# Optimization experiments

Hardware: AMD Instinct MI355X
Metric: run time of the kernel (lower is better)

The kernel has to match this reference:

```python
import jax, jax.numpy as jnp
import numpy as np


def setup_inputs() -> dict:
    key = jax.random.key(0)
    ks = jax.random.split(key, 9)
    b, m, e, d = 4, 4096, 2048, 256
    s = 1.0 / np.sqrt(d)
    return {
        "features": jax.random.normal(ks[0], (b, m, d), jnp.float32),
        "inc_mat": (jax.random.uniform(ks[1], (b, m, e)) < 0.05).astype(jnp.float32),
        "vc_W_att": jax.random.normal(ks[2], (d, d), jnp.float32) * s,
        "vc_W_proj": jax.random.normal(ks[3], (d, d), jnp.float32) * s,
        "vc_alpha": jnp.float32(0.5),
        "ec_W_att": jax.random.normal(ks[4], (d, d), jnp.float32) * s,
        "ec_W_proj": jax.random.normal(ks[5], (d, d), jnp.float32) * s,
        "ec_alpha": jnp.float32(0.5),
        "n_layers": 3,
    }


def _vertex_conv(feat, inc, W_att, W_proj, alpha, prev_edge):
    # feat: [b,m,d], inc: [b,m,e]
    node_scores = jnp.einsum('bmd,kd->bmk', feat, W_att)          # attention Linear (x @ W.T)
    edge_scores = jnp.einsum('bme,bmd->bed', inc, node_scores)    # inc^T @ scores
    attn = jax.nn.softmax(edge_scores, axis=1)                    # softmax over edge dim (dim=1 in torch)
    # einsum('bme,bmd->bmed') then ('bmed,bed->bed') == attn * (inc^T @ feat); no 4D intermediate
    agg = jnp.einsum('bme,bmd->bed', inc, feat)
    ef = jnp.einsum('bed,kd->bek', attn * agg, W_proj)
    if prev_edge is not None:
        ef = alpha * prev_edge + (1.0 - alpha) * ef
    return ef


def _edge_conv(inc, edge_feats, W_proj, alpha, prev_node):
    # note: EdgeConv's attention softmax is computed but unused in the original forward
    weighted = jnp.einsum('bed,bme->bmd', edge_feats, inc)        # scatter edges back to nodes
    nf = jnp.einsum('bmd,kd->bmk', weighted, W_proj)
    if prev_node is not None:
        nf = alpha * prev_node + (1.0 - alpha) * nf
    return nf


def reference(features, inc_mat, vc_W_att, vc_W_proj, vc_alpha, ec_W_att, ec_W_proj, ec_alpha, n_layers):
    edge_feats = _vertex_conv(features, inc_mat, vc_W_att, vc_W_proj, vc_alpha, None)
    node_feats = _edge_conv(inc_mat, edge_feats, ec_W_proj, ec_alpha, features)
    for _ in range(1, int(n_layers)):
        edge_feats = _vertex_conv(features, inc_mat, vc_W_att, vc_W_proj, vc_alpha, edge_feats)
        node_feats = _edge_conv(inc_mat, edge_feats, ec_W_proj, ec_alpha, node_feats)
    return (node_feats, edge_feats, inc_mat)
```

## Files before the change

### kernel.cpp

```cpp
#include <hip/hip_runtime.h>
#include <hip/hip_bf16.h>
#include <math.h>

typedef __attribute__((ext_vector_type(8))) short s8v;
typedef __attribute__((ext_vector_type(4))) float f32x4;

__device__ __forceinline__ ushort f2bf(float x){ __hip_bfloat16 h = __float2bfloat16(x); return *(ushort*)&h; }
__device__ __forceinline__ float  bf2f(ushort u){ return __bfloat162float(*(__hip_bfloat16*)&u); }

__device__ __forceinline__ void gload16(const void* g, void* l) {
  __builtin_amdgcn_global_load_lds(
      (const __attribute__((address_space(1))) void*)g,
      (__attribute__((address_space(3))) void*)l, 16, 0, 0);
}

template<int MAP> __device__ __forceinline__ int kmap(int k){
  if constexpr (MAP==0) return k;
  else if constexpr (MAP==1) return k & 4095;
  else if constexpr (MAP==3) return (((k>>8)&1)<<8) | (k&255);
  else if constexpr (MAP==4) return k & 255;
  else return (((k>>9)&1)<<8) | (k&255);
}

template<int AMAP, int BMAP, int EPI, int FR, int GORD>
__global__ __launch_bounds__(256)
void gemm_kernel(const ushort* __restrict__ A, int lda, long long sA,
                 const ushort* __restrict__ B, int ldb, long long sB,
                 void* __restrict__ Cp, void* __restrict__ Cp2,
                 int ldc, long long sC, int ldc2, long long sC2,
                 long long kpC, int Kloc, int kparts,
                 const float* __restrict__ blend,
                 const float* __restrict__ alpha_p, const int* __restrict__ L_p)
{
  constexpr int BMt = 32*FR;
  __shared__ ushort As[BMt][32];
  __shared__ ushort Bs[BMt][32];

  const int z  = blockIdx.z;
  const int b  = z / kparts;
  const int kp = z - b*kparts;
  const int kbase = kp * Kloc;
  A += (size_t)b * sA;
  B += (size_t)b * sB;
  const int m0 = (GORD ? blockIdx.x : blockIdx.y) * BMt;
  const int n0 = (GORD ? blockIdx.y : blockIdx.x) * BMt;
  const int t = threadIdx.x, lane = t & 63, wid = t >> 6;
  const int wr = (wid>>1)*(16*FR), wc = (wid&1)*(16*FR);
  const int lrow = lane & 15, koff = (lane>>4)<<3;
  const int rsub = lane >> 2;
  const int kc   = (lane & 3) * 8;

  f32x4 acc[FR][FR];
  #pragma unroll
  for (int i=0;i<FR;i++)
    #pragma unroll
    for (int j=0;j<FR;j++) acc[i][j] = (f32x4)(0.f);

  for (int k0 = 0; k0 < Kloc; k0 += 32) {
    #pragma unroll
    for (int c = wid; c < 2*FR; c += 4) {
      const int row = c*16 + rsub;
      gload16(A + (size_t)(m0+row)*lda + kmap<AMAP>(kbase+k0+kc), (char*)&As[0][0] + c*1024);
      gload16(B + (size_t)(n0+row)*ldb + kmap<BMAP>(kbase+k0+kc), (char*)&Bs[0][0] + c*1024);
    }
    __syncthreads();
    s8v af[FR], bfv[FR];
    #pragma unroll
    for (int mi=0; mi<FR; mi++) af[mi]  = *(const s8v*)&As[wr+mi*16+lrow][koff];
    #pragma unroll
    for (int ni=0; ni<FR; ni++) bfv[ni] = *(const s8v*)&Bs[wc+ni*16+lrow][koff];
    #pragma unroll
    for (int mi=0; mi<FR; mi++)
      #pragma unroll
      for (int ni=0; ni<FR; ni++)
        acc[mi][ni] = __builtin_amdgcn_mfma_f32_16x16x32_bf16(af[mi], bfv[ni], acc[mi][ni], 0,0,0);
    __syncthreads();
  }

  float aL = 0.f;
  if constexpr (EPI==2) { aL = powf(*alpha_p, (float)(*L_p)); }
  const int cr = (lane>>4)<<2, cc = lane & 15;
  #pragma unroll
  for (int mi=0; mi<FR; mi++)
    #pragma unroll
    for (int ni=0; ni<FR; ni++) {
      const int row0 = m0 + wr + mi*16 + cr;
      const int col  = n0 + wc + ni*16 + cc;
      if constexpr (EPI==0) {
        float* C = (float*)Cp + kp*kpC + (size_t)b*sC;
        #pragma unroll
        for (int r=0;r<4;r++) C[(size_t)(row0+r)*ldc + col] = acc[mi][ni][r];
      } else if constexpr (EPI==2) {
        float* C = (float*)Cp + (size_t)b*sC;
        const float* bl = blend + (size_t)b*sC;
        #pragma unroll
        for (int r=0;r<4;r++) {
          const size_t idx = (size_t)(row0+r)*ldc + col;
          C[idx] = aL*bl[idx] + (1.f-aL)*acc[mi][ni][r];
        }
      } else if constexpr (EPI==3) {
        float* C = (float*)Cp + (size_t)b*sC;
        ushort* C2 = (ushort*)Cp2 + (size_t)b*sC;
        #pragma unroll
        for (int r=0;r<4;r++) {
          const size_t idx = (size_t)(row0+r)*ldc + col;
          C[idx] = acc[mi][ni][r];
          C2[idx] = f2bf(acc[mi][ni][r]);
        }
      } else if constexpr (EPI==6) {
        float* C = (float*)Cp + (size_t)b*sC;
        #pragma unroll
        for (int r=0;r<4;r++) C[(size_t)(row0+r)*ldc + col] = acc[mi][ni][r];
        float* C2 = (float*)Cp2 + (size_t)b*sC2 + (size_t)col*ldc2 + row0;
        *(f32x4*)C2 = acc[mi][ni];
      } else {
        ushort4 o;
        o.x = f2bf(acc[mi][ni][0]); o.y = f2bf(acc[mi][ni][1]);
        o.z = f2bf(acc[mi][ni][2]); o.w = f2bf(acc[mi][ni][3]);
        *(ushort4*)((ushort*)Cp2 + (size_t)b*sC2 + (size_t)col*ldc2 + row0) = o;
      }
    }
}

__global__ __launch_bounds__(256)
void trans_inc_kernel(const float* __restrict__ src, float* __restrict__ outF32, int writeF32,
                      ushort* __restrict__ incbf, ushort* __restrict__ incT)
{
  __shared__ ushort T[64][65];
  const int b = blockIdx.z, m0 = blockIdx.x*64, e0 = blockIdx.y*64;
  const int t = threadIdx.x, rl = t>>2, cl = (t&3)*16;
  const size_t roff = (size_t)b*4096*2048 + (size_t)(m0+rl)*2048 + e0 + cl;
  const float* s = src + roff;
  ushort tmp[16] __attribute__((aligned(16)));
  float4 vv[4];
  #pragma unroll
  for (int i=0;i<4;i++) {
    vv[i] = ((const float4*)s)[i];
    tmp[4*i+0]=f2bf(vv[i].x); tmp[4*i+1]=f2bf(vv[i].y);
    tmp[4*i+2]=f2bf(vv[i].z); tmp[4*i+3]=f2bf(vv[i].w);
  }
  if (writeF32) {
    float4* o = (float4*)(outF32 + roff);
    #pragma unroll
    for (int i=0;i<4;i++) o[i] = vv[i];
  }
  ushort* d = incbf + roff;
  *(s8v*)d = *(s8v*)&tmp[0]; *(s8v*)(d+8) = *(s8v*)&tmp[8];
  #pragma unroll
  for (int j=0;j<16;j++) T[rl][cl+j] = tmp[j];
  __syncthreads();
  const int er = t>>2, mc = (t&3)*16;
  ushort o[16] __attribute__((aligned(16)));
  #pragma unroll
  for (int j=0;j<16;j++) o[j] = T[mc+j][er];
  ushort* d2 = incT + (size_t)b*2048*4096 + (size_t)(e0+er)*4096 + m0 + mc;
  *(s8v*)d2 = *(s8v*)&o[0]; *(s8v*)(d2+8) = *(s8v*)&o[8];
}

__global__ __launch_bounds__(256)
void trans_feat_kernel(const float* __restrict__ feat, ushort* __restrict__ fT)
{
  __shared__ ushort Th[64][65], Tl[64][65];
  const int b = blockIdx.z, m0 = blockIdx.x*64, d0 = blockIdx.y*64;
  const int t = threadIdx.x, rl = t>>2, cl = (t&3)*16;
  const float* s = feat + (size_t)b*4096*256 + (size_t)(m0+rl)*256 + d0 + cl;
  #pragma unroll
  for (int i=0;i<4;i++) {
    float4 v = ((const float4*)s)[i];
    float a[4] = {v.x,v.y,v.z,v.w};
    #pragma unroll
    for (int j=0;j<4;j++) {
      ushort h = f2bf(a[j]); Th[rl][cl+4*i+j] = h; Tl[rl][cl+4*i+j] = f2bf(a[j] - bf2f(h));
    }
  }
  __syncthreads();
  const int dr = t>>2, mc = (t&3)*16;
  ushort oh[16] __attribute__((aligned(16)));
  ushort ol[16] __attribute__((aligned(16)));
  #pragma unroll
  for (int j=0;j<16;j++) { oh[j] = Th[mc+j][dr]; ol[j] = Tl[mc+j][dr]; }
  ushort* d2 = fT + (size_t)b*256*8192 + (size_t)(d0+dr)*8192 + m0 + mc;
  *(s8v*)d2 = *(s8v*)&oh[0]; *(s8v*)(d2+8) = *(s8v*)&oh[8];
  *(s8v*)(d2+4096) = *(s8v*)&ol[0]; *(s8v*)(d2+4104) = *(s8v*)&ol[8];
}

__global__ __launch_bounds__(256)
void cvt_w_kernel(const float4* __restrict__ W, ushort* __restrict__ Ws)
{
  size_t i  = (size_t)blockIdx.x * 256 + threadIdx.x;
  size_t e0 = i * 4;
  int c = (int)(e0 & 255), r = (int)(e0 >> 8);
  float4 v = W[i];
  float a[4] = {v.x,v.y,v.z,v.w};
  ushort* hi = Ws + (size_t)r*512 + c;
  #pragma unroll
  for (int j=0;j<4;j++) { ushort h = f2bf(a[j]); hi[j] = h; hi[256+j] = f2bf(a[j]-bf2f(h)); }
}

__global__ __launch_bounds__(256)
void aggsum_kernel(const float* __restrict__ parts, long long kpC, int kparts,
                   ushort* __restrict__ AGGcat)
{
  const size_t i4 = (size_t)blockIdx.x*256 + threadIdx.x;
  float4 sv = make_float4(0.f,0.f,0.f,0.f);
  for (int kp=0; kp<kparts; kp++) {
    float4 v = ((const float4*)(parts + (size_t)kp*kpC))[i4];
    sv.x+=v.x; sv.y+=v.y; sv.z+=v.z; sv.w+=v.w;
  }
  const size_t flat = i4*4;
  const size_t row = flat >> 8;
  const int d = (int)(flat & 255);
  float a[4] = {sv.x, sv.y, sv.z, sv.w};
  ushort4 hi, lo;
  { ushort h=f2bf(a[0]); hi.x=h; lo.x=f2bf(a[0]-bf2f(h)); }
  { ushort h=f2bf(a[1]); hi.y=h; lo.y=f2bf(a[1]-bf2f(h)); }
  { ushort h=f2bf(a[2]); hi.z=h; lo.z=f2bf(a[2]-bf2f(h)); }
  { ushort h=f2bf(a[3]); hi.w=h; lo.w=f2bf(a[3]-bf2f(h)); }
  ushort* dst = AGGcat + row*512 + d;
  *(ushort4*)dst = hi; *(ushort4*)(dst+256) = lo;
}

__global__ __launch_bounds__(256)
void stats_kernel(const float* __restrict__ ESt, float2* __restrict__ stats)
{
  const int b = blockIdx.x >> 8, d = blockIdx.x & 255;
  const float* base = ESt + ((size_t)b*256 + d)*2048;
  const int t = threadIdx.x;
  const float4* p = (const float4*)base + t*2;
  float4 x = p[0], y = p[1];
  float v[8] = {x.x,x.y,x.z,x.w,y.x,y.y,y.z,y.w};
  float mx = v[0];
  #pragma unroll
  for (int j=1;j<8;j++) mx = fmaxf(mx, v[j]);
  #pragma unroll
  for (int off=32; off>=1; off>>=1) mx = fmaxf(mx, __shfl_down(mx, off));
  __shared__ float sm[8];
  const int lane = t & 63, w = t >> 6;
  if (lane==0) sm[w] = mx;
  __syncthreads();
  if (t==0) { sm[4] = fmaxf(fmaxf(sm[0],sm[1]),fmaxf(sm[2],sm[3])); }
  __syncthreads();
  mx = sm[4];
  float s = 0.f;
  #pragma unroll
  for (int j=0;j<8;j++) s += __expf(v[j]-mx);
  #pragma unroll
  for (int off=32; off>=1; off>>=1) s += __shfl_down(s, off);
  if (lane==0) sm[w] = s;
  __syncthreads();
  if (t==0) { float ss = sm[0]+sm[1]+sm[2]+sm[3]; stats[blockIdx.x] = make_float2(mx, 1.f/ss); }
}

__global__ __launch_bounds__(256)
void pmul_kernel(const float* __restrict__ ES, const ushort* __restrict__ AGGcat,
                 const float2* __restrict__ stats, ushort* __restrict__ P)
{
  const int b = blockIdx.x >> 6, e0 = (blockIdx.x & 63) * 32;
  const int t = threadIdx.x, tx = t & 63, ty = t >> 6;
  const int d4 = tx*4;
  const float2 st0 = stats[b*256+d4+0], st1 = stats[b*256+d4+1];
  const float2 st2 = stats[b*256+d4+2], st3 = stats[b*256+d4+3];
  for (int e = e0+ty; e < e0+32; e += 4) {
    const size_t ro = (size_t)b*2048 + e;
    float4 es = *(const float4*)(ES + ro*256 + d4);
    ushort4 ah = *(const ushort4*)(AGGcat + ro*512 + d4);
    ushort4 al = *(const ushort4*)(AGGcat + ro*512 + 256 + d4);
    ushort4 o;
    o.x = f2bf(__expf(es.x-st0.x)*st0.y*(bf2f(ah.x)+bf2f(al.x)));
    o.y = f2bf(__expf(es.y-st1.x)*st1.y*(bf2f(ah.y)+bf2f(al.y)));
    o.z = f2bf(__expf(es.z-st2.x)*st2.y*(bf2f(ah.z)+bf2f(al.z)));
    o.w = f2bf(__expf(es.w-st3.x)*st3.y*(bf2f(ah.w)+bf2f(al.w)));
    *(ushort4*)(P + ro*256 + d4) = o;
  }
}

__global__ __launch_bounds__(256)
void inc_copy_kernel(const float4* __restrict__ src, float4* __restrict__ dst, size_t n4)
{
  size_t i = (size_t)blockIdx.x*256 + threadIdx.x;
  const size_t stride = (size_t)gridDim.x*256;
  for (; i < n4; i += stride) dst[i] = src[i];
}

extern "C" void kernel_launch(void* const* d_in, const int* in_sizes, int n_in,
                              void* d_out, int out_size, void* d_ws, size_t ws_size,
                              hipStream_t stream) {
  const float* feat    = (const float*)d_in[0];
  const float* inc     = (const float*)d_in[1];
  const float* vcWatt  = (const float*)d_in[2];
  const float* vcWproj = (const float*)d_in[3];
  const float* ecWproj = (const float*)d_in[6];
  const float* ecAlpha = (const float*)d_in[7];
  const int*   nLayers = (const int*)d_in[8];

  const int Bb=4, Mm=4096, E=2048, D=256;
  const size_t nodeN = (size_t)Bb*Mm*D, edgeN = (size_t)Bb*E*D, incN = (size_t)Bb*Mm*E;

  const int kparts = 8;
  const size_t fTB    = (size_t)Bb*256*8192*2;
  const size_t partsB = (size_t)kparts*Bb*E*D*4;
  const size_t AGGcatB= (size_t)Bb*E*512*2;
  const size_t ESB    = (size_t)Bb*E*D*4;
  const size_t EStB   = ESB;
  const size_t PB     = edgeN*2;
  const size_t ebfB   = edgeN*2;
  const size_t E2TB   = edgeN*2;
  const size_t WsB    = (size_t)3*256*512*2;
  const size_t statB  = (size_t)Bb*256*sizeof(float2);
  const size_t incTB  = incN*2, incbfB = incN*2;
  const size_t needB  = fTB+partsB+AGGcatB+ESB+EStB+PB+ebfB+E2TB+WsB+statB;
  const bool planA = ws_size >= needB + incTB + incbfB;

  char* ws = (char*)d_ws;
  ushort* fT    = (ushort*)ws;  ws += fTB;
  float*  parts = (float*)ws;   ws += partsB;
  ushort* AGGcat= (ushort*)ws;  ws += AGGcatB;
  float*  ES    = (float*)ws;   ws += ESB;
  float*  ESt   = (float*)ws;   ws += EStB;
  ushort* P     = (ushort*)ws;  ws += PB;
  ushort* edgebf= (ushort*)ws;  ws += ebfB;
  ushort* E2T   = (ushort*)ws;  ws += E2TB;
  ushort* Ws0   = (ushort*)ws;
  ushort* Ws1   = Ws0 + 256*512;
  ushort* Ws2   = Ws1 + 256*512;
  ws += WsB;
  float2* stats = (float2*)ws;  ws += statB;

  float* outNode = (float*)d_out;
  float* outEdge = outNode + nodeN;
  float* outInc  = outEdge + edgeN;
  ushort *incT, *incbf;
  if (planA) { incT = (ushort*)ws; incbf = incT + incN; }
  else       { incT = (ushort*)outInc; incbf = incT + incN; }

  const long long kpC = (long long)Bb*E*D;
  dim3 blk(256);

  cvt_w_kernel<<<dim3(64), blk, 0, stream>>>((const float4*)vcWatt,  Ws0);
  cvt_w_kernel<<<dim3(64), blk, 0, stream>>>((const float4*)vcWproj, Ws1);
  cvt_w_kernel<<<dim3(64), blk, 0, stream>>>((const float4*)ecWproj, Ws2);
  trans_feat_kernel<<<dim3(64,4,4), blk, 0, stream>>>(feat, fT);
  trans_inc_kernel<<<dim3(64,32,4), blk, 0, stream>>>(inc, outInc, planA ? 1 : 0, incbf, incT);

  gemm_kernel<1,0,0,4,0><<<dim3(2,16,4*kparts), blk, 0, stream>>>(
      incT, 4096, (long long)E*4096, fT, 8192, (long long)256*8192,
      parts, nullptr, D, (long long)E*D, 0, 0, kpC, 8192/kparts, kparts,
      nullptr, nullptr, nullptr);

  aggsum_kernel<<<dim3(2048), blk, 0, stream>>>(parts, kpC, kparts, AGGcat);

  gemm_kernel<5,3,6,2,0><<<dim3(4,32,4), blk, 0, stream>>>(
      AGGcat, 512, (long long)E*512, Ws0, 512, 0,
      ES, ESt, D, (long long)E*D, E, (long long)D*E, 0, 1024, 1,
      nullptr, nullptr, nullptr);

  stats_kernel<<<dim3(Bb*256), blk, 0, stream>>>(ESt, stats);
  pmul_kernel<<<dim3(Bb*64), blk, 0, stream>>>(ES, AGGcat, stats, P);

  gemm_kernel<4,3,3,2,0><<<dim3(4,32,4), blk, 0, stream>>>(
      P, 256, (long long)E*D, Ws1, 512, 0,
      outEdge, edgebf, D, (long long)E*D, 0, 0, 0, 512, 1,
      nullptr, nullptr, nullptr);

  gemm_kernel<4,3,8,2,0><<<dim3(4,32,4), blk, 0, stream>>>(
      edgebf, 256, (long long)E*D, Ws2, 512, 0,
      nullptr, E2T, D, (long long)E*D, E, (long long)D*E, 0, 512, 1,
      nullptr, nullptr, nullptr);

  gemm_kernel<0,0,2,2,1><<<dim3(64,4,4), blk, 0, stream>>>(
      incbf, 2048, (long long)Mm*E, E2T, 2048, (long long)D*E,
      outNode, nullptr, D, (long long)Mm*D, 0, 0, 0, 2048, 1,
      feat, ecAlpha, nLayers);

  if (!planA)
    inc_copy_kernel<<<dim3(2048), blk, 0, stream>>>((const float4*)inc, (float4*)outInc, incN/4);
}
```

Measured before the change: 512.1 us.

## Fold hi/lo split into interleaved rows instead of split-K for aggregation GEMM

New measurement: 541.4 us. +5.7%, slower.

```diff
diff --git a/kernel.cpp b/kernel.cpp
--- a/kernel.cpp
+++ b/kernel.cpp
@@ -16,7 +16,6 @@
 
 template<int MAP> __device__ __forceinline__ int kmap(int k){
   if constexpr (MAP==0) return k;
-  else if constexpr (MAP==1) return k & 4095;
   else if constexpr (MAP==3) return (((k>>8)&1)<<8) | (k&255);
   else if constexpr (MAP==4) return k & 255;
   else return (((k>>9)&1)<<8) | (k&255);
@@ -28,7 +27,7 @@
                  const ushort* __restrict__ B, int ldb, long long sB,
                  void* __restrict__ Cp, void* __restrict__ Cp2,
                  int ldc, long long sC, int ldc2, long long sC2,
-                 long long kpC, int Kloc, int kparts,
+                 int Kloc,
                  const float* __restrict__ blend,
                  const float* __restrict__ alpha_p, const int* __restrict__ L_p)
 {
@@ -36,10 +35,7 @@
   __shared__ ushort As[BMt][32];
   __shared__ ushort Bs[BMt][32];
 
-  const int z  = blockIdx.z;
-  const int b  = z / kparts;
-  const int kp = z - b*kparts;
-  const int kbase = kp * Kloc;
+  const int b = blockIdx.z;
   A += (size_t)b * sA;
   B += (size_t)b * sB;
   const int m0 = (GORD ? blockIdx.x : blockIdx.y) * BMt;
@@ -60,8 +56,8 @@
     #pragma unroll
     for (int c = wid; c < 2*FR; c += 4) {
       const int row = c*16 + rsub;
-      gload16(A + (size_t)(m0+row)*lda + kmap<AMAP>(kbase+k0+kc), (char*)&As[0][0] + c*1024);
-      gload16(B + (size_t)(n0+row)*ldb + kmap<BMAP>(kbase+k0+kc), (char*)&Bs[0][0] + c*1024);
+      gload16(A + (size_t)(m0+row)*lda + kmap<AMAP>(k0+kc), (char*)&As[0][0] + c*1024);
+      gload16(B + (size_t)(n0+row)*ldb + kmap<BMAP>(k0+kc), (char*)&Bs[0][0] + c*1024);
     }
     __syncthreads();
     s8v af[FR], bfv[FR];
@@ -86,11 +82,7 @@
     for (int ni=0; ni<FR; ni++) {
       const int row0 = m0 + wr + mi*16 + cr;
       const int col  = n0 + wc + ni*16 + cc;
-      if constexpr (EPI==0) {
-        float* C = (float*)Cp + kp*kpC + (size_t)b*sC;
-        #pragma unroll
-        for (int r=0;r<4;r++) C[(size_t)(row0+r)*ldc + col] = acc[mi][ni][r];
-      } else if constexpr (EPI==2) {
+      if constexpr (EPI==2) {
         float* C = (float*)Cp + (size_t)b*sC;
         const float* bl = blend + (size_t)b*sC;
         #pragma unroll
@@ -113,11 +105,16 @@
         for (int r=0;r<4;r++) C[(size_t)(row0+r)*ldc + col] = acc[mi][ni][r];
         float* C2 = (float*)Cp2 + (size_t)b*sC2 + (size_t)col*ldc2 + row0;
         *(f32x4*)C2 = acc[mi][ni];
-      } else {
+      } else if constexpr (EPI==8) {
         ushort4 o;
         o.x = f2bf(acc[mi][ni][0]); o.y = f2bf(acc[mi][ni][1]);
         o.z = f2bf(acc[mi][ni][2]); o.w = f2bf(acc[mi][ni][3]);
         *(ushort4*)((ushort*)Cp2 + (size_t)b*sC2 + (size_t)col*ldc2 + row0) = o;
+      } else {
+        float* C = (float*)Cp + (size_t)b*sC;
+        const int d0 = row0 >> 1;
+        C[(size_t)d0*ldc + col]     = acc[mi][ni][0] + acc[mi][ni][1];
+        C[(size_t)(d0+1)*ldc + col] = acc[mi][ni][2] + acc[mi][ni][3];
       }
     }
 }
@@ -158,7 +155,7 @@
 }
 
 __global__ __launch_bounds__(256)
-void trans_feat_kernel(const float* __restrict__ feat, ushort* __restrict__ fT)
+void trans_feat_kernel(const float* __restrict__ feat, ushort* __restrict__ fTi)
 {
   __shared__ ushort Th[64][65], Tl[64][65];
   const int b = blockIdx.z, m0 = blockIdx.x*64, d0 = blockIdx.y*64;
@@ -179,9 +176,36 @@
   ushort ol[16] __attribute__((aligned(16)));
   #pragma unroll
   for (int j=0;j<16;j++) { oh[j] = Th[mc+j][dr]; ol[j] = Tl[mc+j][dr]; }
-  ushort* d2 = fT + (size_t)b*256*8192 + (size_t)(d0+dr)*8192 + m0 + mc;
+  ushort* d2 = fTi + (size_t)b*512*4096 + (size_t)(2*(d0+dr))*4096 + m0 + mc;
   *(s8v*)d2 = *(s8v*)&oh[0]; *(s8v*)(d2+8) = *(s8v*)&oh[8];
   *(s8v*)(d2+4096) = *(s8v*)&ol[0]; *(s8v*)(d2+4104) = *(s8v*)&ol[8];
+}
+
+__global__ __launch_bounds__(256)
+void aggt2cat_kernel(const float* __restrict__ AGGT, ushort* __restrict__ AGGcat)
+{
+  __shared__ ushort Th[64][65], Tl[64][65];
+  const int b = blockIdx.z, d0 = blockIdx.x*64, e0 = blockIdx.y*64;
+  const int t = threadIdx.x, rl = t>>2, cl = (t&3)*16;
+  const float* s = AGGT + (size_t)b*256*2048 + (size_t)(d0+rl)*2048 + e0 + cl;
+  #pragma unroll
+  for (int i=0;i<4;i++) {
+    float4 v = ((const float4*)s)[i];
+    float a[4] = {v.x,v.y,v.z,v.w};
+    #pragma unroll
+    for (int j=0;j<4;j++) {
+      ushort h = f2bf(a[j]); Th[rl][cl+4*i+j] = h; Tl[rl][cl+4*i+j] = f2bf(a[j] - bf2f(h));
+    }
+  }
+  __syncthreads();
+  const int er = t>>2, dc = (t&3)*16;
+  ushort oh[16] __attribute__((aligned(16)));
+  ushort ol[16] __attribute__((aligned(16)));
+  #pragma unroll
+  for (int j=0;j<16;j++) { oh[j] = Th[dc+j][er]; ol[j] = Tl[dc+j][er]; }
+  ushort* d2 = AGGcat + ((size_t)b*2048 + e0 + er)*512 + d0 + dc;
+  *(s8v*)d2 = *(s8v*)&oh[0]; *(s8v*)(d2+8) = *(s8v*)&oh[8];
+  *(s8v*)(d2+256) = *(s8v*)&ol[0]; *(s8v*)(d2+264) = *(s8v*)&ol[8];
 }
 
 __global__ __launch_bounds__(256)
@@ -195,29 +219,6 @@
   ushort* hi = Ws + (size_t)r*512 + c;
   #pragma unroll
   for (int j=0;j<4;j++) { ushort h = f2bf(a[j]); hi[j] = h; hi[256+j] = f2bf(a[j]-bf2f(h)); }
-}
-
-__global__ __launch_bounds__(256)
-void aggsum_kernel(const float* __restrict__ parts, long long kpC, int kparts,
-                   ushort* __restrict__ AGGcat)
-{
-  const size_t i4 = (size_t)blockIdx.x*256 + threadIdx.x;
-  float4 sv = make_float4(0.f,0.f,0.f,0.f);
-  for (int kp=0; kp<kparts; kp++) {
-    float4 v = ((const float4*)(parts + (size_t)kp*kpC))[i4];
-    sv.x+=v.x; sv.y+=v.y; sv.z+=v.z; sv.w+=v.w;
-  }
-  const size_t flat = i4*4;
-  const size_t row = flat >> 8;
-  const int d = (int)(flat & 255);
-  float a[4] = {sv.x, sv.y, sv.z, sv.w};
-  ushort4 hi, lo;
-  { ushort h=f2bf(a[0]); hi.x=h; lo.x=f2bf(a[0]-bf2f(h)); }
-  { ushort h=f2bf(a[1]); hi.y=h; lo.y=f2bf(a[1]-bf2f(h)); }
-  { ushort h=f2bf(a[2]); hi.z=h; lo.z=f2bf(a[2]-bf2f(h)); }
-  { ushort h=f2bf(a[3]); hi.w=h; lo.w=f2bf(a[3]-bf2f(h)); }
-  ushort* dst = AGGcat + row*512 + d;
-  *(ushort4*)dst = hi; *(ushort4*)(dst+256) = lo;
 }
 
 __global__ __launch_bounds__(256)
@@ -296,9 +297,8 @@
   const int Bb=4, Mm=4096, E=2048, D=256;
   const size_t nodeN = (size_t)Bb*Mm*D, edgeN = (size_t)Bb*E*D, incN = (size_t)Bb*Mm*E;
 
-  const int kparts = 8;
-  const size_t fTB    = (size_t)Bb*256*8192*2;
-  const size_t partsB = (size_t)kparts*Bb*E*D*4;
+  const size_t fTiB   = (size_t)Bb*512*4096*2;
+  const size_t AGGTB  = (size_t)Bb*256*2048*4;
   const size_t AGGcatB= (size_t)Bb*E*512*2;
   const size_t ESB    = (size_t)Bb*E*D*4;
   const size_t EStB   = ESB;
@@ -308,12 +308,12 @@
   const size_t WsB    = (size_t)3*256*512*2;
   const size_t statB  = (size_t)Bb*256*sizeof(float2);
   const size_t incTB  = incN*2, incbfB = incN*2;
-  const size_t needB  = fTB+partsB+AGGcatB+ESB+EStB+PB+ebfB+E2TB+WsB+statB;
+  const size_t needB  = fTiB+AGGTB+AGGcatB+ESB+EStB+PB+ebfB+E2TB+WsB+statB;
   const bool planA = ws_size >= needB + incTB + incbfB;
 
   char* ws = (char*)d_ws;
-  ushort* fT    = (ushort*)ws;  ws += fTB;
-  float*  parts = (float*)ws;   ws += partsB;
+  ushort* fTi   = (ushort*)ws;  ws += fTiB;
+  float*  AGGT  = (float*)ws;   ws += AGGTB;
   ushort* AGGcat= (ushort*)ws;  ws += AGGcatB;
   float*  ES    = (float*)ws;   ws += ESB;
   float*  ESt   = (float*)ws;   ws += EStB;
@@ -333,25 +333,24 @@
   if (planA) { incT = (ushort*)ws; incbf = incT + incN; }
   else       { incT = (ushort*)outInc; incbf = incT + incN; }
 
-  const long long kpC = (long long)Bb*E*D;
   dim3 blk(256);
 
   cvt_w_kernel<<<dim3(64), blk, 0, stream>>>((const float4*)vcWatt,  Ws0);
   cvt_w_kernel<<<dim3(64), blk, 0, stream>>>((const float4*)vcWproj, Ws1);
   cvt_w_kernel<<<dim3(64), blk, 0, stream>>>((const float4*)ecWproj, Ws2);
-  trans_feat_kernel<<<dim3(64,4,4), blk, 0, stream>>>(feat, fT);
+  trans_feat_kernel<<<dim3(64,4,4), blk, 0, stream>>>(feat, fTi);
   trans_inc_kernel<<<dim3(64,32,4), blk, 0, stream>>>(inc, outInc, planA ? 1 : 0, incbf, incT);
 
-  gemm_kernel<1,0,0,4,0><<<dim3(2,16,4*kparts), blk, 0, stream>>>(
-      incT, 4096, (long long)E*4096, fT, 8192, (long long)256*8192,
-      parts, nullptr, D, (long long)E*D, 0, 0, kpC, 8192/kparts, kparts,
+  gemm_kernel<0,0,9,4,0><<<dim3(16,4,4), blk, 0, stream>>>(
+      fTi, 4096, (long long)512*4096, incT, 4096, (long long)E*4096,
+      AGGT, nullptr, E, (long long)D*E, 0, 0, 4096,
       nullptr, nullptr, nullptr);
 
-  aggsum_kernel<<<dim3(2048), blk, 0, stream>>>(parts, kpC, kparts, AGGcat);
+  aggt2cat_kernel<<<dim3(4,32,4), blk, 0, stream>>>(AGGT, AGGcat);
 
   gemm_kernel<5,3,6,2,0><<<dim3(4,32,4), blk, 0, stream>>>(
       AGGcat, 512, (long long)E*512, Ws0, 512, 0,
-      ES, ESt, D, (long long)E*D, E, (long long)D*E, 0, 1024, 1,
+      ES, ESt, D, (long long)E*D, E, (long long)D*E, 1024,
       nullptr, nullptr, nullptr);
 
   stats_kernel<<<dim3(Bb*256), blk, 0, stream>>>(ESt, stats);
@@ -359,17 +358,17 @@
 
   gemm_kernel<4,3,3,2,0><<<dim3(4,32,4), blk, 0, stream>>>(
       P, 256, (long long)E*D, Ws1, 512, 0,
-      outEdge, edgebf, D, (long long)E*D, 0, 0, 0, 512, 1,
+      outEdge, edgebf, D, (long long)E*D, 0, 0, 512,
       nullptr, nullptr, nullptr);
 
   gemm_kernel<4,3,8,2,0><<<dim3(4,32,4), blk, 0, stream>>>(
       edgebf, 256, (long long)E*D, Ws2, 512, 0,
-      nullptr, E2T, D, (long long)E*D, E, (long long)D*E, 0, 512, 1,
+      nullptr, E2T, D, (long long)E*D, E, (long long)D*E, 512,
       nullptr, nullptr, nullptr);
 
   gemm_kernel<0,0,2,2,1><<<dim3(64,4,4), blk, 0, stream>>>(
       incbf, 2048, (long long)Mm*E, E2T, 2048, (long long)D*E,
-      outNode, nullptr, D, (long long)Mm*D, 0, 0, 0, 2048, 1,
+      outNode, nullptr, D, (long long)Mm*D, 0, 0, 2048,
       feat, ecAlpha, nLayers);
 
   if (!planA)
```
